# Performance work log

Measured on AMD Instinct MI355X. Metric: run time of the kernel, lower is better.

The kernel has to match this reference:

```python
import jax, jax.numpy as jnp
import numpy as np

B, IMG, P, D, HEADS, DEPTH = 8, 384, 16, 768, 12, 12
HD = D // HEADS  # 64
EPS = 1e-5


def _ln(x, s, b):
    m = x.mean(-1, keepdims=True)
    v = ((x - m) ** 2).mean(-1, keepdims=True)
    return (x - m) / jnp.sqrt(v + EPS) * s + b


def _rotate_half(x):
    x1, x2 = jnp.split(x, 2, axis=-1)
    return jnp.concatenate([-x2, x1], axis=-1)


def _build_2d_rope(gh, gw, hd):
    half = hd // 2
    inv_freq = 1.0 / (10000.0 ** (jnp.arange(0, half, 2, dtype=jnp.float32) / half))  # [hd//4]
    yf = jnp.arange(gh, dtype=jnp.float32)[:, None] * inv_freq[None, :]  # [gh, hd//4]
    xf = jnp.arange(gw, dtype=jnp.float32)[:, None] * inv_freq[None, :]  # [gw, hd//4]
    yf = jnp.broadcast_to(yf[:, None, :], (gh, gw, half // 2))
    xf = jnp.broadcast_to(xf[None, :, :], (gh, gw, half // 2))
    comb = jnp.concatenate([yf, xf], axis=-1)          # [gh, gw, hd//2]
    comb = jnp.repeat(comb, 2, axis=-1)                # [gh, gw, hd]
    return jnp.sin(comb).reshape(-1, hd), jnp.cos(comb).reshape(-1, hd)


def _forward(x, patch_w, patch_b, cls_token, ln1_s, ln1_b, qkv_w, proj_w, proj_b,
             ln2_s, ln2_b, mlp_w1, mlp_b1, mlp_w2, mlp_b2, norm_s, norm_b):
    Bb, _, H, W = x.shape
    gh, gw = H // P, W // P
    # patch embed: Conv2d(3, D, P, stride=P) == reshape to patches + matmul
    patches = x.reshape(Bb, 3, gh, P, gw, P).transpose(0, 2, 4, 1, 3, 5).reshape(Bb, gh * gw, 3 * P * P)
    t = patches @ patch_w.reshape(D, -1).T + patch_b  # [B, L0, D]
    sin, cos = _build_2d_rope(gh, gw, HD)             # [L0, HD]
    t = jnp.concatenate([jnp.broadcast_to(cls_token, (Bb, 1, D)), t], axis=1)  # [B, L, D]
    L = t.shape[1]
    scale = HD ** -0.5
    sin_b = sin[None, None]  # [1,1,L0,HD]
    cos_b = cos[None, None]

    def rope(u):
        return u * cos_b + _rotate_half(u) * sin_b

    for i in range(DEPTH):
        h = _ln(t, ln1_s[i], ln1_b[i])
        qkv = (h @ qkv_w[i].T).reshape(Bb, L, 3, HEADS, HD).transpose(2, 0, 3, 1, 4)
        q, k, v = qkv[0], qkv[1], qkv[2]  # [B, H, L, HD]
        # RoPE on patch tokens only (CLS token untouched)
        q = jnp.concatenate([q[:, :, :1], rope(q[:, :, 1:])], axis=2)
        k = jnp.concatenate([k[:, :, :1], rope(k[:, :, 1:])], axis=2)
        attn = jnp.einsum('bhqd,bhkd->bhqk', q, k) * scale
        attn = jax.nn.softmax(attn, axis=-1)
        o = jnp.einsum('bhqk,bhkd->bhqd', attn, v).transpose(0, 2, 1, 3).reshape(Bb, L, D)
        t = t + o @ proj_w[i].T + proj_b[i]
        h2 = _ln(t, ln2_s[i], ln2_b[i])
        t = t + jax.nn.gelu(h2 @ mlp_w1[i].T + mlp_b1[i], approximate=False) @ mlp_w2[i].T + mlp_b2[i]

    return _ln(t[:, 0], norm_s, norm_b)  # [B, D]


def setup_inputs() -> dict:
    key = jax.random.key(0)
    ks = jax.random.split(key, 8)
    s = 0.02
    HID = 4 * D
    return {
        'x': jax.random.normal(ks[0], (B, 3, IMG, IMG), jnp.float32),
        'patch_w': jax.random.normal(ks[1], (D, 3, P, P), jnp.float32) * s,
        'patch_b': jnp.zeros((D,), jnp.float32),
        'cls_token': jnp.zeros((1, 1, D), jnp.float32),
        'ln1_s': jnp.ones((DEPTH, D), jnp.float32),
        'ln1_b': jnp.zeros((DEPTH, D), jnp.float32),
        'qkv_w': jax.random.normal(ks[2], (DEPTH, 3 * D, D), jnp.float32) * s,
        'proj_w': jax.random.normal(ks[3], (DEPTH, D, D), jnp.float32) * s,
        'proj_b': jnp.zeros((DEPTH, D), jnp.float32),
        'ln2_s': jnp.ones((DEPTH, D), jnp.float32),
        'ln2_b': jnp.zeros((DEPTH, D), jnp.float32),
        'mlp_w1': jax.random.normal(ks[4], (DEPTH, HID, D), jnp.float32) * s,
        'mlp_b1': jnp.zeros((DEPTH, HID), jnp.float32),
        'mlp_w2': jax.random.normal(ks[5], (DEPTH, D, HID), jnp.float32) * s,
        'mlp_b2': jnp.zeros((DEPTH, D), jnp.float32),
        'norm_s': jnp.ones((D,), jnp.float32),
        'norm_b': jnp.zeros((D,), jnp.float32),
    }


def reference(x, patch_w, patch_b, cls_token, ln1_s, ln1_b, qkv_w, proj_w, proj_b,
              ln2_s, ln2_b, mlp_w1, mlp_b1, mlp_w2, mlp_b2, norm_s, norm_b):
    return _forward(x, patch_w, patch_b, cls_token, ln1_s, ln1_b, qkv_w, proj_w, proj_b,
                    ln2_s, ln2_b, mlp_w1, mlp_b1, mlp_w2, mlp_b2, norm_s, norm_b)
```

## Files before the change

kernel.cpp:

```cpp
#include <hip/hip_runtime.h>
#include <math.h>

#define NB 8
#define DDIM 768
#define NHEAD 12
#define NDEPTH 12
#define HDIM 64
#define GRIDW 24
#define NL0 576
#define NL 577
#define LPAD 640
#define NHID 3072
#define MROWS (NB*NL)
#define MPAD 4736
#define EPSV 1e-5f
#define QT2 5
#define NCONV 512

typedef unsigned short ushortT;
typedef __attribute__((ext_vector_type(8))) short bf16x8;
typedef __attribute__((ext_vector_type(4))) float f32x4;

__device__ __forceinline__ ushortT f2b(float f) {
    union { float f; unsigned u; } x; x.f = f;
    unsigned r = x.u + 0x7fffu + ((x.u >> 16) & 1u);
    return (ushortT)(r >> 16);
}

__device__ __forceinline__ float b2f(ushortT u) {
    union { unsigned u; float f; } x; x.u = ((unsigned)u) << 16;
    return x.f;
}

__device__ __forceinline__ void load_lds16(const void* g, void* l) {
    __builtin_amdgcn_global_load_lds((const __attribute__((address_space(1))) void*)g,
                                     (__attribute__((address_space(3))) void*)l, 16, 0, 0);
}

__global__ void f2b_k(const float* __restrict__ in, ushortT* __restrict__ out, long n) {
    for (long i = ((long)blockIdx.x * 256 + threadIdx.x) * 4; i < n; i += (long)gridDim.x * 1024) {
        float4 v = *(const float4*)(in + i);
        ushort4 o; o.x = f2b(v.x); o.y = f2b(v.y); o.z = f2b(v.z); o.w = f2b(v.w);
        *(ushort4*)(out + i) = o;
    }
}

__global__ void wconv4_k(const float* __restrict__ a, ushortT* __restrict__ ao, long na,
                         const float* __restrict__ b, ushortT* __restrict__ bo, long nb,
                         const float* __restrict__ c, ushortT* __restrict__ co, long nc,
                         const float* __restrict__ d, ushortT* __restrict__ dd, long nd) {
    long stride = (long)gridDim.x * 1024;
    long i0 = ((long)blockIdx.x * 256 + threadIdx.x) * 4;
    for (long i = i0; i < na; i += stride) {
        float4 v = *(const float4*)(a + i);
        ushort4 o; o.x = f2b(v.x); o.y = f2b(v.y); o.z = f2b(v.z); o.w = f2b(v.w);
        *(ushort4*)(ao + i) = o;
    }
    for (long i = i0; i < nb; i += stride) {
        float4 v = *(const float4*)(b + i);
        ushort4 o; o.x = f2b(v.x); o.y = f2b(v.y); o.z = f2b(v.z); o.w = f2b(v.w);
        *(ushort4*)(bo + i) = o;
    }
    for (long i = i0; i < nc; i += stride) {
        float4 v = *(const float4*)(c + i);
        ushort4 o; o.x = f2b(v.x); o.y = f2b(v.y); o.z = f2b(v.z); o.w = f2b(v.w);
        *(ushort4*)(co + i) = o;
    }
    for (long i = i0; i < nd; i += stride) {
        float4 v = *(const float4*)(d + i);
        ushort4 o; o.x = f2b(v.x); o.y = f2b(v.y); o.z = f2b(v.z); o.w = f2b(v.w);
        *(ushort4*)(dd + i) = o;
    }
}

__global__ void im2col_k(const float* __restrict__ x, ushortT* __restrict__ p) {
    for (long idx = (long)blockIdx.x * 256 + threadIdx.x; idx < (long)4608 * 768; idx += (long)gridDim.x * 256) {
        int row = (int)(idx / 768), col = (int)(idx - (long)row * 768);
        int b = row / NL0, pi = row - b * NL0;
        int gy = pi / GRIDW, gx = pi - gy * GRIDW;
        int c = col >> 8, r = col & 255;
        int py = r >> 4, px = r & 15;
        p[idx] = f2b(x[(((long)(b * 3 + c) * 384) + gy * 16 + py) * 384 + gx * 16 + px]);
    }
}

__global__ void cls_k(const float* __restrict__ cls, float* __restrict__ t) {
    t[(long)blockIdx.x * NL * DDIM + threadIdx.x] = cls[threadIdx.x];
}

__global__ void rope_k(float* __restrict__ sin_t, float* __restrict__ cos_t) {
    int pos = blockIdx.x, d = threadIdx.x;
    int gy = pos / GRIDW, gx = pos - gy * GRIDW;
    int j = d >> 1;
    float ang;
    if (j < 16) ang = (float)gy * powf(10000.f, -(float)j / 16.f);
    else        ang = (float)gx * powf(10000.f, -(float)(j - 16) / 16.f);
    sin_t[pos * 64 + d] = sinf(ang);
    cos_t[pos * 64 + d] = cosf(ang);
}

__global__ __launch_bounds__(256) void ln_k(const float* __restrict__ in,
                                            const float* __restrict__ sc,
                                            const float* __restrict__ bi,
                                            float* __restrict__ outf,
                                            ushortT* __restrict__ outb,
                                            long in_rstride) {
    int row = blockIdx.x;
    const float* ip = in + (long)row * in_rstride;
    float x[3];
    float s = 0.f, s2 = 0.f;
    #pragma unroll
    for (int i = 0; i < 3; ++i) {
        x[i] = ip[threadIdx.x + i * 256];
        s += x[i]; s2 += x[i] * x[i];
    }
    __shared__ float red0[256], red1[256];
    red0[threadIdx.x] = s; red1[threadIdx.x] = s2;
    __syncthreads();
    for (int off = 128; off; off >>= 1) {
        if (threadIdx.x < off) {
            red0[threadIdx.x] += red0[threadIdx.x + off];
            red1[threadIdx.x] += red1[threadIdx.x + off];
        }
        __syncthreads();
    }
    float mean = red0[0] * (1.f / 768.f);
    float var  = red1[0] * (1.f / 768.f) - mean * mean;
    float inv = rsqrtf(var + EPSV);
    #pragma unroll
    for (int i = 0; i < 3; ++i) {
        int c = threadIdx.x + i * 256;
        float val = (x[i] - mean) * inv * sc[c] + bi[c];
        if (outb) outb[(long)row * 768 + c] = f2b(val);
        else      outf[(long)row * 768 + c] = val;
    }
}

__global__ __launch_bounds__(256) void red_ln_k(const ushortT* __restrict__ psum,
                                                const float* __restrict__ b2,
                                                float* __restrict__ t,
                                                const float* __restrict__ sc,
                                                const float* __restrict__ bi,
                                                ushortT* __restrict__ outb) {
    int row = blockIdx.x;
    const size_t S = (size_t)MPAD * DDIM;
    const size_t rb = (size_t)row * DDIM;
    float x[3];
    float s = 0.f, s2 = 0.f;
    #pragma unroll
    for (int i = 0; i < 3; ++i) {
        int c = threadIdx.x + i * 256;
        float v = t[rb + c] + b2[c] + b2f(psum[rb + c]) + b2f(psum[S + rb + c])
                + b2f(psum[2 * S + rb + c]) + b2f(psum[3 * S + rb + c]);
        x[i] = v; s += v; s2 += v * v;
        t[rb + c] = v;
    }
    __shared__ float red0[256], red1[256];
    red0[threadIdx.x] = s; red1[threadIdx.x] = s2;
    __syncthreads();
    for (int off = 128; off; off >>= 1) {
        if (threadIdx.x < off) {
            red0[threadIdx.x] += red0[threadIdx.x + off];
            red1[threadIdx.x] += red1[threadIdx.x + off];
        }
        __syncthreads();
    }
    float mean = red0[0] * (1.f / 768.f);
    float var  = red1[0] * (1.f / 768.f) - mean * mean;
    float inv = rsqrtf(var + EPSV);
    #pragma unroll
    for (int i = 0; i < 3; ++i) {
        int c = threadIdx.x + i * 256;
        outb[rb + c] = f2b((x[i] - mean) * inv * sc[c] + bi[c]);
    }
}

__global__ __launch_bounds__(256) void red_final_k(const ushortT* __restrict__ psum,
                                                   const float* __restrict__ b2,
                                                   const float* __restrict__ t,
                                                   const float* __restrict__ sc,
                                                   const float* __restrict__ bi,
                                                   float* __restrict__ outf) {
    int row = blockIdx.x * NL;
    const size_t S = (size_t)MPAD * DDIM;
    const size_t rb = (size_t)row * DDIM;
    float x[3];
    float s = 0.f, s2 = 0.f;
    #pragma unroll
    for (int i = 0; i < 3; ++i) {
        int c = threadIdx.x + i * 256;
        float v = t[rb + c] + b2[c] + b2f(psum[rb + c]) + b2f(psum[S + rb + c])
                + b2f(psum[2 * S + rb + c]) + b2f(psum[3 * S + rb + c]);
        x[i] = v; s += v; s2 += v * v;
    }
    __shared__ float red0[256], red1[256];
    red0[threadIdx.x] = s; red1[threadIdx.x] = s2;
    __syncthreads();
    for (int off = 128; off; off >>= 1) {
        if (threadIdx.x < off) {
            red0[threadIdx.x] += red0[threadIdx.x + off];
            red1[threadIdx.x] += red1[threadIdx.x + off];
        }
        __syncthreads();
    }
    float mean = red0[0] * (1.f / 768.f);
    float var  = red1[0] * (1.f / 768.f) - mean * mean;
    float inv = rsqrtf(var + EPSV);
    #pragma unroll
    for (int i = 0; i < 3; ++i) {
        int c = threadIdx.x + i * 256;
        outf[(long)blockIdx.x * 768 + c] = (x[i] - mean) * inv * sc[c] + bi[c];
    }
}

template<int WR, int WC, int MI, int NI, int SPLITK, int NW>
__global__ __launch_bounds__(NW * 64) void gemm_t(const ushortT* __restrict__ A,
                                                  const ushortT* __restrict__ W,
                                                  const float* __restrict__ bias,
                                                  const float* __restrict__ resid,
                                                  float* __restrict__ Cf,
                                                  ushortT* __restrict__ Cb,
                                                  const float* __restrict__ sinT,
                                                  const float* __restrict__ cosT,
                                                  ushortT* __restrict__ qo,
                                                  ushortT* __restrict__ ko,
                                                  ushortT* __restrict__ vo,
                                                  ushortT* __restrict__ psum,
                                                  int N, int K, int flags) {
    constexpr int BM = WR * MI * 16;
    constexpr int BN = WC * NI * 16;
    constexpr int THREADS = NW * 64;
    constexpr int ACH = (BM * 64) / (THREADS * 8);
    constexpr int BCH = (BN * 64) / (THREADS * 8);
    __shared__ ushortT As[2][BM * 64];
    __shared__ ushortT Bs[2][BN * 64];
    int tid = threadIdx.x;
    int lane = tid & 63, wid = tid >> 6;
    int wm = wid / WC, wn = wid % WC;
    int lr = lane & 15, lk = lane >> 4;
    int nwg = gridDim.x * gridDim.y;
    int flat = blockIdx.y * gridDim.x + blockIdx.x;
    int qq = nwg >> 3, rr = nwg & 7;
    int xcd = flat & 7, idx = flat >> 3;
    int wg = (xcd < rr ? xcd * (qq + 1) : rr * (qq + 1) + (xcd - rr) * qq) + idx;
    int bx = wg % gridDim.x, by = wg / gridDim.x;
    int m0 = by * BM, n0 = bx * BN;
    int kspan = K / SPLITK;
    int k0 = (SPLITK > 1) ? blockIdx.z * kspan : 0;
    f32x4 acc[MI][NI] = {};

    auto stage = [&](int buf, int kt) {
        #pragma unroll
        for (int i = 0; i < ACH; ++i) {
            int ch = i * THREADS + tid;
            int r = ch >> 3, cb = (ch & 7) * 16;
            int cbs = cb ^ ((r & 7) << 4);
            load_lds16(A + (size_t)(m0 + r) * K + kt + (cbs >> 1), &As[buf][ch * 8]);
        }
        #pragma unroll
        for (int i = 0; i < BCH; ++i) {
            int ch = i * THREADS + tid;
            int r = ch >> 3, cb = (ch & 7) * 16;
            int cbs = cb ^ ((r & 7) << 4);
            load_lds16(W + (size_t)(n0 + r) * K + kt + (cbs >> 1), &Bs[buf][ch * 8]);
        }
    };

    stage(0, k0);
    asm volatile("s_waitcnt vmcnt(0)" ::: "memory");
    __builtin_amdgcn_s_barrier();
    int nk = kspan / 64;
    int cur = 0;
    for (int it = 0; it < nk; ++it) {
        if (it + 1 < nk) stage(cur ^ 1, k0 + (it + 1) * 64);
        #pragma unroll
        for (int ks = 0; ks < 2; ++ks) {
            bf16x8 aF[MI], bF[NI];
            #pragma unroll
            for (int mi = 0; mi < MI; ++mi) {
                int row = wm * MI * 16 + mi * 16 + lr;
                aF[mi] = *(const bf16x8*)((const char*)&As[cur][0] + row * 128 +
                                          ((ks * 64 + lk * 16) ^ ((row & 7) << 4)));
            }
            #pragma unroll
            for (int ni = 0; ni < NI; ++ni) {
                int row = wn * NI * 16 + ni * 16 + lr;
                bF[ni] = *(const bf16x8*)((const char*)&Bs[cur][0] + row * 128 +
                                          ((ks * 64 + lk * 16) ^ ((row & 7) << 4)));
            }
            #pragma unroll
            for (int mi = 0; mi < MI; ++mi)
                #pragma unroll
                for (int ni = 0; ni < NI; ++ni)
                    acc[mi][ni] = __builtin_amdgcn_mfma_f32_16x16x32_bf16(aF[mi], bF[ni], acc[mi][ni], 0, 0, 0);
        }
        asm volatile("s_waitcnt vmcnt(0)" ::: "memory");
        __builtin_amdgcn_s_barrier();
        cur ^= 1;
    }

    if (SPLITK > 1) {
        #pragma unroll
        for (int mi = 0; mi < MI; ++mi) {
            int rbase = m0 + wm * MI * 16 + mi * 16 + (lane >> 4) * 4;
            #pragma unroll
            for (int ni = 0; ni < NI; ++ni) {
                int c = n0 + wn * NI * 16 + ni * 16 + lr;
                #pragma unroll
                for (int r = 0; r < 4; ++r)
                    psum[((size_t)blockIdx.z * MPAD + rbase + r) * N + c] = f2b(acc[mi][ni][r]);
            }
        }
        return;
    }
    if (flags & 64) {
        if constexpr (NI == 4 && BN == 128) {
            int selB = n0 / DDIM;
            if (selB == 2) {
                ushortT* vtile = &As[0][0];
                #pragma unroll
                for (int mi = 0; mi < MI; ++mi) {
                    #pragma unroll
                    for (int ni = 0; ni < NI; ++ni) {
                        #pragma unroll
                        for (int r = 0; r < 4; ++r) {
                            int ll = wm * MI * 16 + mi * 16 + (lane >> 4) * 4 + r;
                            int dl = wn * 64 + ni * 16 + lr;
                            vtile[dl * BM + (ll ^ ((dl & 7) << 4))] = f2b(acc[mi][ni][r]);
                        }
                    }
                }
                __syncthreads();
                for (int e = tid; e < 128 * BM; e += THREADS) {
                    int dl = e / BM, ll = e - dl * BM;
                    int row = m0 + ll;
                    if (row < MROWS) {
                        int b = row / NL, l = row - b * NL;
                        int cv = (n0 - 2 * DDIM) + dl;
                        int h = cv >> 6, d = cv & 63;
                        int bh = b * NHEAD + h;
                        vo[((long)bh * HDIM + d) * LPAD + l] = vtile[dl * BM + (ll ^ ((dl & 7) << 4))];
                    }
                }
            } else {
                #pragma unroll
                for (int mi = 0; mi < MI; ++mi) {
                    #pragma unroll
                    for (int r = 0; r < 4; ++r) {
                        int row = m0 + wm * MI * 16 + mi * 16 + (lane >> 4) * 4 + r;
                        if (row >= MROWS) continue;
                        int b = row / NL, l = row - b * NL;
                        #pragma unroll
                        for (int ni = 0; ni < NI; ++ni) {
                            int c = n0 + wn * 64 + ni * 16 + lr;
                            float val = acc[mi][ni][r];
                            int sel = c / DDIM;
                            int cc = c - sel * DDIM;
                            int h = cc >> 6, d = cc & 63;
                            if (l > 0) {
                                int pos = l - 1;
                                float cs = cosT[pos * 64 + d], sn = sinT[pos * 64 + d];
                                float partner = acc[mi][ni ^ 2][r];
                                float rh = (d < 32) ? -partner : partner;
                                val = val * cs + rh * sn;
                            }
                            int bh = b * NHEAD + h;
                            if (sel == 0) qo[((long)bh * LPAD + l) * HDIM + d] = f2b(val * 0.125f);
                            else          ko[((long)bh * LPAD + l) * HDIM + d] = f2b(val);
                        }
                    }
                }
            }
        }
        return;
    }
    #pragma unroll
    for (int mi = 0; mi < MI; ++mi) {
        int rbase = m0 + wm * MI * 16 + mi * 16 + (lane >> 4) * 4;
        #pragma unroll
        for (int ni = 0; ni < NI; ++ni) {
            int c = n0 + wn * NI * 16 + ni * 16 + lr;
            float bv = (flags & 1) ? bias[c] : 0.f;
            #pragma unroll
            for (int r = 0; r < 4; ++r) {
                int row = rbase + r;
                float val = acc[mi][ni][r] + bv;
                if (flags & 4) val = 0.5f * val * (1.f + erff(val * 0.70710678118654752f));
                long orow = row;
                if (flags & 8) orow = (long)(row / NL0) * NL + 1 + (row % NL0);
                if (flags & 2) val += resid[orow * (long)N + c];
                if (flags & 16) Cf[orow * (long)N + c] = val;
                if (flags & 32) Cb[orow * (long)N + c] = f2b(val);
            }
        }
    }
}

__global__ __launch_bounds__(256) void fattn_k(const ushortT* __restrict__ q,
                                               const ushortT* __restrict__ k,
                                               const ushortT* __restrict__ vt,
                                               ushortT* __restrict__ o,
                                               const float* __restrict__ wa, ushortT* __restrict__ wao, long na,
                                               const float* __restrict__ wb, ushortT* __restrict__ wbo, long nbn,
                                               const float* __restrict__ wc, ushortT* __restrict__ wco, long nc,
                                               const float* __restrict__ wd, ushortT* __restrict__ wdo, long nd) {
    if (blockIdx.x >= 96 * QT2) {
        int cid = blockIdx.x - 96 * QT2;
        long stride = (long)NCONV * 1024;
        long i0 = ((long)cid * 256 + threadIdx.x) * 4;
        for (long i = i0; i < na; i += stride) {
            float4 v = *(const float4*)(wa + i);
            ushort4 t4; t4.x = f2b(v.x); t4.y = f2b(v.y); t4.z = f2b(v.z); t4.w = f2b(v.w);
            *(ushort4*)(wao + i) = t4;
        }
        for (long i = i0; i < nbn; i += stride) {
            float4 v = *(const float4*)(wb + i);
            ushort4 t4; t4.x = f2b(v.x); t4.y = f2b(v.y); t4.z = f2b(v.z); t4.w = f2b(v.w);
            *(ushort4*)(wbo + i) = t4;
        }
        for (long i = i0; i < nc; i += stride) {
            float4 v = *(const float4*)(wc + i);
            ushort4 t4; t4.x = f2b(v.x); t4.y = f2b(v.y); t4.z = f2b(v.z); t4.w = f2b(v.w);
            *(ushort4*)(wco + i) = t4;
        }
        for (long i = i0; i < nd; i += stride) {
            float4 v = *(const float4*)(wd + i);
            ushort4 t4; t4.x = f2b(v.x); t4.y = f2b(v.y); t4.z = f2b(v.z); t4.w = f2b(v.w);
            *(ushort4*)(wdo + i) = t4;
        }
        return;
    }
    __shared__ ushortT Qs[2][4096], Ks[4096], Vs[4096], Ps[4096];
    int tid = threadIdx.x;
    int wave = tid >> 6, lane = tid & 63;
    int lr = lane & 15, lk = lane >> 4, g = lk;
    int bh = blockIdx.x / QT2, qp = blockIdx.x % QT2;
    int q0 = qp * 128;
    int b = bh / NHEAD, h = bh - b * NHEAD;
    int l8 = lane >> 3, c16 = lane & 7;
    int colsw = (c16 * 16) ^ ((l8 & 7) << 4);

    #pragma unroll
    for (int qs = 0; qs < 2; ++qs) {
        const ushortT* src = q + ((long)bh * LPAD + q0 + qs * 64) * HDIM;
        #pragma unroll
        for (int j = 0; j < 2; ++j) {
            int row = wave * 16 + j * 8 + l8;
            load_lds16(src + (long)row * HDIM + (colsw >> 1), Qs[qs] + wave * 1024 + j * 512);
        }
    }
    __syncthreads();
    bf16x8 qF[2][2];
    #pragma unroll
    for (int qs = 0; qs < 2; ++qs)
        #pragma unroll
        for (int ks = 0; ks < 2; ++ks) {
            int row = wave * 16 + lr;
            qF[qs][ks] = *(const bf16x8*)((const char*)Qs[qs] + row * 128 +
                                          ((ks * 64 + lk * 16) ^ ((lr & 7) << 4)));
        }
    f32x4 oa[2][4] = {};
    float m_r[2][4], l_r[2][4];
    #pragma unroll
    for (int qs = 0; qs < 2; ++qs)
        #pragma unroll
        for (int r = 0; r < 4; ++r) { m_r[qs][r] = -3e38f; l_r[qs][r] = 0.f; }

    for (int t0 = 0; t0 < 10; ++t0) {
        int k0 = t0 * 64;
        __syncthreads();
        {
            const ushortT* srck = k + ((long)bh * LPAD + k0) * HDIM;
            const ushortT* srcv = vt + (long)bh * HDIM * LPAD + k0;
            #pragma unroll
            for (int j = 0; j < 2; ++j) {
                int row = wave * 16 + j * 8 + l8;
                load_lds16(srck + (long)row * HDIM + (colsw >> 1), Ks + wave * 1024 + j * 512);
                load_lds16(srcv + (long)row * LPAD + (colsw >> 1), Vs + wave * 1024 + j * 512);
            }
        }
        __syncthreads();
        #pragma unroll
        for (int qs = 0; qs < 2; ++qs) {
            f32x4 s[4] = {};
            #pragma unroll
            for (int ks = 0; ks < 2; ++ks) {
                #pragma unroll
                for (int kt = 0; kt < 4; ++kt) {
                    int row = kt * 16 + lr;
                    bf16x8 kF = *(const bf16x8*)((const char*)Ks + row * 128 +
                                                 ((ks * 64 + lk * 16) ^ ((lr & 7) << 4)));
                    s[kt] = __builtin_amdgcn_mfma_f32_16x16x32_bf16(qF[qs][ks], kF, s[kt], 0, 0, 0);
                }
            }
            if (k0 + 63 > 576) {
                #pragma unroll
                for (int kt = 0; kt < 4; ++kt)
                    if (k0 + kt * 16 + lr > 576) {
                        #pragma unroll
                        for (int r = 0; r < 4; ++r) s[kt][r] = -3e38f;
                    }
            }
            float mx[4], al[4], rs[4];
            #pragma unroll
            for (int r = 0; r < 4; ++r)
                mx[r] = fmaxf(fmaxf(s[0][r], s[1][r]), fmaxf(s[2][r], s[3][r]));
            #pragma unroll
            for (int off = 1; off < 16; off <<= 1) {
                #pragma unroll
                for (int r = 0; r < 4; ++r) mx[r] = fmaxf(mx[r], __shfl_xor(mx[r], off));
            }
            #pragma unroll
            for (int r = 0; r < 4; ++r) {
                float mn = fmaxf(m_r[qs][r], mx[r]);
                al[r] = __expf(m_r[qs][r] - mn);
                m_r[qs][r] = mn;
                rs[r] = 0.f;
            }
            #pragma unroll
            for (int kt = 0; kt < 4; ++kt) {
                #pragma unroll
                for (int r = 0; r < 4; ++r) {
                    float p = __expf(s[kt][r] - m_r[qs][r]);
                    rs[r] += p;
                    int rowp = g * 4 + r;
                    *(ushortT*)((char*)Ps + wave * 2048 + rowp * 128 +
                                ((kt * 32 + lr * 2) ^ ((rowp & 7) << 4))) = f2b(p);
                }
            }
            #pragma unroll
            for (int off = 1; off < 16; off <<= 1) {
                #pragma unroll
                for (int r = 0; r < 4; ++r) rs[r] += __shfl_xor(rs[r], off);
            }
            #pragma unroll
            for (int r = 0; r < 4; ++r) l_r[qs][r] = l_r[qs][r] * al[r] + rs[r];
            #pragma unroll
            for (int dt = 0; dt < 4; ++dt) {
                #pragma unroll
                for (int r = 0; r < 4; ++r) oa[qs][dt][r] *= al[r];
            }
            #pragma unroll
            for (int ks = 0; ks < 2; ++ks) {
                bf16x8 pA = *(const bf16x8*)((const char*)Ps + wave * 2048 + lr * 128 +
                                             ((ks * 64 + lk * 16) ^ ((lr & 7) << 4)));
                #pragma unroll
                for (int dt = 0; dt < 4; ++dt) {
                    bf16x8 vF = *(const bf16x8*)((const char*)Vs + (dt * 16 + lr) * 128 +
                                                 ((ks * 64 + lk * 16) ^ ((lr & 7) << 4)));
                    oa[qs][dt] = __builtin_amdgcn_mfma_f32_16x16x32_bf16(pA, vF, oa[qs][dt], 0, 0, 0);
                }
            }
        }
    }
    #pragma unroll
    for (int qs = 0; qs < 2; ++qs) {
        #pragma unroll
        for (int r = 0; r < 4; ++r) {
            int l = q0 + qs * 64 + wave * 16 + g * 4 + r;
            if (l > 576) continue;
            float inv = 1.f / l_r[qs][r];
            #pragma unroll
            for (int dt = 0; dt < 4; ++dt)
                o[((long)(b * NL + l)) * DDIM + h * HDIM + dt * 16 + lr] = f2b(oa[qs][dt][r] * inv);
        }
    }
}

extern "C" void kernel_launch(void* const* d_in, const int* in_sizes, int n_in,
                              void* d_out, int out_size, void* d_ws, size_t ws_size,
                              hipStream_t stream) {
    const float* x       = (const float*)d_in[0];
    const float* patch_w = (const float*)d_in[1];
    const float* patch_b = (const float*)d_in[2];
    const float* cls     = (const float*)d_in[3];
    const float* ln1_s   = (const float*)d_in[4];
    const float* ln1_b   = (const float*)d_in[5];
    const float* qkv_w   = (const float*)d_in[6];
    const float* proj_w  = (const float*)d_in[7];
    const float* proj_b  = (const float*)d_in[8];
    const float* ln2_s   = (const float*)d_in[9];
    const float* ln2_b   = (const float*)d_in[10];
    const float* mlp_w1  = (const float*)d_in[11];
    const float* mlp_b1  = (const float*)d_in[12];
    const float* mlp_w2  = (const float*)d_in[13];
    const float* mlp_b2  = (const float*)d_in[14];
    const float* norm_s  = (const float*)d_in[15];
    const float* norm_b  = (const float*)d_in[16];

    const size_t SZ_WQ = (size_t)3 * DDIM * DDIM;
    const size_t SZ_WP = (size_t)DDIM * DDIM;
    const size_t SZ_W1 = (size_t)NHID * DDIM;
    const size_t SZ_W2 = (size_t)DDIM * NHID;

    char* w = (char*)d_ws;
    float* t      = (float*)w;  w += (size_t)MPAD * DDIM * 4;
    float* sin_t  = (float*)w;  w += (size_t)NL0 * HDIM * 4;
    float* cos_t  = (float*)w;  w += (size_t)NL0 * HDIM * 4;
    ushortT* psum = (ushortT*)w; w += (size_t)4 * MPAD * DDIM * 2;
    ushortT* h_bf   = (ushortT*)w; w += (size_t)MPAD * DDIM * 2;
    ushortT* o_bf   = (ushortT*)w; w += (size_t)MPAD * DDIM * 2;
    ushortT* mlp_bf = (ushortT*)w; w += (size_t)MPAD * NHID * 2;
    ushortT* patches = mlp_bf;
    ushortT* q_bf   = (ushortT*)w; w += (size_t)96 * LPAD * HDIM * 2;
    ushortT* k_bf   = (ushortT*)w; w += (size_t)96 * LPAD * HDIM * 2;
    ushortT* v_t    = (ushortT*)w; w += (size_t)96 * HDIM * LPAD * 2;
    ushortT* pw_bf  = (ushortT*)w; w += (size_t)DDIM * 768 * 2;
    ushortT* wqB[2]; ushortT* wpB[2]; ushortT* w1B[2]; ushortT* w2B[2];
    for (int s = 0; s < 2; ++s) {
        wqB[s] = (ushortT*)w; w += SZ_WQ * 2;
        wpB[s] = (ushortT*)w; w += SZ_WP * 2;
        w1B[s] = (ushortT*)w; w += SZ_W1 * 2;
        w2B[s] = (ushortT*)w; w += SZ_W2 * 2;
    }

    const float* nfp = nullptr;
    ushortT* nus = nullptr;
    float* nf = nullptr;

    hipLaunchKernelGGL(rope_k, dim3(NL0), dim3(64), 0, stream, sin_t, cos_t);
    hipLaunchKernelGGL(im2col_k, dim3(2048), dim3(256), 0, stream, x, patches);
    hipLaunchKernelGGL(f2b_k, dim3(512), dim3(256), 0, stream, patch_w, pw_bf, (long)DDIM * 768);
    hipLaunchKernelGGL(cls_k, dim3(NB), dim3(DDIM), 0, stream, cls, t);
    hipLaunchKernelGGL(wconv4_k, dim3(1024), dim3(256), 0, stream,
                       qkv_w, wqB[0], (long)SZ_WQ,
                       proj_w, wpB[0], (long)SZ_WP,
                       mlp_w1, w1B[0], (long)SZ_W1,
                       mlp_w2, w2B[0], (long)SZ_W2);
    hipLaunchKernelGGL((gemm_t<2, 4, 2, 2, 1, 8>), dim3(DDIM / 128, 4608 / 64), dim3(512), 0, stream,
                       patches, pw_bf, patch_b, nfp, t, nus, nfp, nfp, nus, nus, nus, nus,
                       DDIM, 768, 1 | 8 | 16);

    for (int i = 0; i < NDEPTH; ++i) {
        int cur = i & 1, nxt = (i + 1) & 1;
        if (i == 0) {
            hipLaunchKernelGGL(ln_k, dim3(MROWS), dim3(256), 0, stream,
                               t, ln1_s, ln1_b, nf, h_bf, (long)DDIM);
        } else {
            hipLaunchKernelGGL(red_ln_k, dim3(MROWS), dim3(256), 0, stream,
                               psum, mlp_b2 + (i - 1) * DDIM, t,
                               ln1_s + i * DDIM, ln1_b + i * DDIM, h_bf);
        }
        hipLaunchKernelGGL((gemm_t<4, 2, 2, 4, 1, 8>), dim3((3 * DDIM) / 128, MPAD / 128), dim3(512), 0, stream,
                           h_bf, wqB[cur], nfp, nfp, nf, nus, sin_t, cos_t,
                           q_bf, k_bf, v_t, nus, 3 * DDIM, DDIM, 64);
        long cn = (i + 1 < NDEPTH) ? 1 : 0;
        hipLaunchKernelGGL(fattn_k, dim3(96 * QT2 + NCONV), dim3(256), 0, stream,
                           q_bf, k_bf, v_t, o_bf,
                           qkv_w + SZ_WQ * (i + 1), wqB[nxt], cn * (long)SZ_WQ,
                           proj_w + SZ_WP * (i + 1), wpB[nxt], cn * (long)SZ_WP,
                           mlp_w1 + SZ_W1 * (i + 1), w1B[nxt], cn * (long)SZ_W1,
                           mlp_w2 + SZ_W2 * (i + 1), w2B[nxt], cn * (long)SZ_W2);
        hipLaunchKernelGGL((gemm_t<2, 4, 2, 2, 1, 8>), dim3(DDIM / 128, MPAD / 64), dim3(512), 0, stream,
                           o_bf, wpB[cur], proj_b + i * DDIM, t, t, nus, nfp, nfp, nus, nus, nus, nus,
                           DDIM, DDIM, 1 | 2 | 16);
        hipLaunchKernelGGL(ln_k, dim3(MROWS), dim3(256), 0, stream,
                           t, ln2_s + i * DDIM, ln2_b + i * DDIM, nf, h_bf, (long)DDIM);
        hipLaunchKernelGGL((gemm_t<4, 2, 2, 4, 1, 8>), dim3(NHID / 128, MPAD / 128), dim3(512), 0, stream,
                           h_bf, w1B[cur], mlp_b1 + i * NHID, nfp, nf, mlp_bf, nfp, nfp,
                           nus, nus, nus, nus, NHID, DDIM, 1 | 4 | 32);
        hipLaunchKernelGGL((gemm_t<4, 2, 2, 4, 4, 8>), dim3(DDIM / 128, MPAD / 128, 4), dim3(512), 0, stream,
                           mlp_bf, w2B[cur], nfp, nfp, nf, nus, nfp, nfp,
                           nus, nus, nus, psum, DDIM, NHID, 0);
    }
    hipLaunchKernelGGL(red_final_k, dim3(NB), dim3(256), 0, stream,
                       psum, mlp_b2 + (NDEPTH - 1) * DDIM, t, norm_s, norm_b, (float*)d_out);
}
```

Baseline: 2.360 ms.

## Widen attention blocks to 512 threads covering 256 queries per K/V tile

The flash-attention kernel now runs 8 waves per block, and each block handles 256 query rows instead of 128, so the grid drops from 5 to 3 query tiles per batch-head. Each K/V tile loaded into LDS is now reused by twice as many query rows. The loads are split so one group of four waves fetches K and the other fetches V. The trade-off is fewer, larger blocks: query tiles past the padded length sit idle in the last block per head, and the smaller grid may fit the CU count less evenly. The fused weight-conversion blocks are resized to the new thread count.

After: 2.545 ms. +7.8%, slower.

```diff
diff --git a/kernel.cpp b/kernel.cpp
--- a/kernel.cpp
+++ b/kernel.cpp
@@ -14,7 +14,7 @@
 #define MROWS (NB*NL)
 #define MPAD 4736
 #define EPSV 1e-5f
-#define QT2 5
+#define QT3 3
 #define NCONV 512
 
 typedef unsigned short ushortT;
@@ -396,7 +396,7 @@
     }
 }
 
-__global__ __launch_bounds__(256) void fattn_k(const ushortT* __restrict__ q,
+__global__ __launch_bounds__(512) void fattn_k(const ushortT* __restrict__ q,
                                                const ushortT* __restrict__ k,
                                                const ushortT* __restrict__ vt,
                                                ushortT* __restrict__ o,
@@ -404,10 +404,10 @@
                                                const float* __restrict__ wb, ushortT* __restrict__ wbo, long nbn,
                                                const float* __restrict__ wc, ushortT* __restrict__ wco, long nc,
                                                const float* __restrict__ wd, ushortT* __restrict__ wdo, long nd) {
-    if (blockIdx.x >= 96 * QT2) {
-        int cid = blockIdx.x - 96 * QT2;
-        long stride = (long)NCONV * 1024;
-        long i0 = ((long)cid * 256 + threadIdx.x) * 4;
+    if (blockIdx.x >= 96 * QT3) {
+        int cid = blockIdx.x - 96 * QT3;
+        long stride = (long)NCONV * 2048;
+        long i0 = ((long)cid * 512 + threadIdx.x) * 4;
         for (long i = i0; i < na; i += stride) {
             float4 v = *(const float4*)(wa + i);
             ushort4 t4; t4.x = f2b(v.x); t4.y = f2b(v.y); t4.z = f2b(v.z); t4.w = f2b(v.w);
@@ -430,23 +430,29 @@
         }
         return;
     }
-    __shared__ ushortT Qs[2][4096], Ks[4096], Vs[4096], Ps[4096];
+    __shared__ ushortT Qs[4][4096], Ks[4096], Vs[4096];
+    __shared__ ushortT Ps[8192];
     int tid = threadIdx.x;
     int wave = tid >> 6, lane = tid & 63;
+    int g2 = wave >> 2, wavein = wave & 3;
     int lr = lane & 15, lk = lane >> 4, g = lk;
-    int bh = blockIdx.x / QT2, qp = blockIdx.x % QT2;
-    int q0 = qp * 128;
+    int bh = blockIdx.x / QT3, qp = blockIdx.x % QT3;
+    int q0 = qp * 256;
     int b = bh / NHEAD, h = bh - b * NHEAD;
     int l8 = lane >> 3, c16 = lane & 7;
     int colsw = (c16 * 16) ^ ((l8 & 7) << 4);
 
     #pragma unroll
     for (int qs = 0; qs < 2; ++qs) {
-        const ushortT* src = q + ((long)bh * LPAD + q0 + qs * 64) * HDIM;
-        #pragma unroll
-        for (int j = 0; j < 2; ++j) {
-            int row = wave * 16 + j * 8 + l8;
-            load_lds16(src + (long)row * HDIM + (colsw >> 1), Qs[qs] + wave * 1024 + j * 512);
+        int tileq = g2 * 2 + qs;
+        int start = q0 + tileq * 64;
+        if (start < LPAD) {
+            const ushortT* src = q + ((long)bh * LPAD + start) * HDIM;
+            #pragma unroll
+            for (int j = 0; j < 2; ++j) {
+                int row = wavein * 16 + j * 8 + l8;
+                load_lds16(src + (long)row * HDIM + (colsw >> 1), Qs[tileq] + wavein * 1024 + j * 512);
+            }
         }
     }
     __syncthreads();
@@ -455,8 +461,8 @@
     for (int qs = 0; qs < 2; ++qs)
         #pragma unroll
         for (int ks = 0; ks < 2; ++ks) {
-            int row = wave * 16 + lr;
-            qF[qs][ks] = *(const bf16x8*)((const char*)Qs[qs] + row * 128 +
+            int row = wavein * 16 + lr;
+            qF[qs][ks] = *(const bf16x8*)((const char*)Qs[g2 * 2 + qs] + row * 128 +
                                           ((ks * 64 + lk * 16) ^ ((lr & 7) << 4)));
         }
     f32x4 oa[2][4] = {};
@@ -470,18 +476,23 @@
         int k0 = t0 * 64;
         __syncthreads();
         {
-            const ushortT* srck = k + ((long)bh * LPAD + k0) * HDIM;
-            const ushortT* srcv = vt + (long)bh * HDIM * LPAD + k0;
             #pragma unroll
             for (int j = 0; j < 2; ++j) {
-                int row = wave * 16 + j * 8 + l8;
-                load_lds16(srck + (long)row * HDIM + (colsw >> 1), Ks + wave * 1024 + j * 512);
-                load_lds16(srcv + (long)row * LPAD + (colsw >> 1), Vs + wave * 1024 + j * 512);
+                int row = wavein * 16 + j * 8 + l8;
+                if (g2 == 0) {
+                    const ushortT* srck = k + ((long)bh * LPAD + k0) * HDIM;
+                    load_lds16(srck + (long)row * HDIM + (colsw >> 1), Ks + wavein * 1024 + j * 512);
+                } else {
+                    const ushortT* srcv = vt + (long)bh * HDIM * LPAD + k0;
+                    load_lds16(srcv + (long)row * LPAD + (colsw >> 1), Vs + wavein * 1024 + j * 512);
+                }
             }
         }
         __syncthreads();
         #pragma unroll
         for (int qs = 0; qs < 2; ++qs) {
+            int start = q0 + (g2 * 2 + qs) * 64;
+            if (start > 576) continue;
             f32x4 s[4] = {};
             #pragma unroll
             for (int ks = 0; ks < 2; ++ks) {
@@ -557,7 +568,7 @@
     for (int qs = 0; qs < 2; ++qs) {
         #pragma unroll
         for (int r = 0; r < 4; ++r) {
-            int l = q0 + qs * 64 + wave * 16 + g * 4 + r;
+            int l = q0 + (g2 * 2 + qs) * 64 + wavein * 16 + g * 4 + r;
             if (l > 576) continue;
             float inv = 1.f / l_r[qs][r];
             #pragma unroll
@@ -645,7 +656,7 @@
                            h_bf, wqB[cur], nfp, nfp, nf, nus, sin_t, cos_t,
                            q_bf, k_bf, v_t, nus, 3 * DDIM, DDIM, 64);
         long cn = (i + 1 < NDEPTH) ? 1 : 0;
-        hipLaunchKernelGGL(fattn_k, dim3(96 * QT2 + NCONV), dim3(256), 0, stream,
+        hipLaunchKernelGGL(fattn_k, dim3(96 * QT3 + NCONV), dim3(512), 0, stream,
                            q_bf, k_bf, v_t, o_bf,
                            qkv_w + SZ_WQ * (i + 1), wqB[nxt], cn * (long)SZ_WQ,
                            proj_w + SZ_WP * (i + 1), wpB[nxt], cn * (long)SZ_WP,
```
